# Kernel optimization log

Hardware: AMD Instinct MI355X
Metric: run time of the kernel (lower is better)

## Reference

```python
import jax, jax.numpy as jnp
import numpy as np

B, N, D_IN = 8, 1024, 512
H, D_HEAD = 8, 64
D_EXPAND, D_OUT = 2048, 512
D_Q = D_HEAD * H            # 512
D_V = D_IN * H              # 4096
D_QKV = 2 * D_Q + D_V       # 5120
EPS = 1e-5


def setup_inputs() -> dict:
    key = jax.random.key(0)
    ks = jax.random.split(key, 16)
    s = 0.02
    return {
        "x": jax.random.normal(ks[0], (B, N, D_IN), jnp.float32),
        "pos_enc": jax.random.normal(ks[1], (1, N, D_IN), jnp.float32),
        "gamma1": jnp.ones((1, 1, D_IN), jnp.float32),
        "beta1": jnp.zeros((1, 1, D_IN), jnp.float32),
        "scale": jnp.asarray(1.414, jnp.float32),
        "W_qkv": jax.random.normal(ks[2], (D_IN, D_QKV), jnp.float32) * s,
        "b_qkv": jax.random.normal(ks[3], (D_QKV,), jnp.float32) * s,
        "W_merge": jax.random.normal(ks[4], (D_V, D_IN), jnp.float32) * s,
        "b_merge": jax.random.normal(ks[5], (D_IN,), jnp.float32) * s,
        "gamma2": jnp.ones((1, 1, D_IN), jnp.float32),
        "beta2": jnp.zeros((1, 1, D_IN), jnp.float32),
        "W1": jax.random.normal(ks[6], (D_IN, D_EXPAND), jnp.float32) * s,
        "b1": jax.random.normal(ks[7], (D_EXPAND,), jnp.float32) * s,
        "gamma3": jnp.ones((1, 1, D_EXPAND), jnp.float32),
        "beta3": jnp.zeros((1, 1, D_EXPAND), jnp.float32),
        "W2": jax.random.normal(ks[8], (D_EXPAND, D_OUT), jnp.float32) * s,
        "b2": jax.random.normal(ks[9], (D_OUT,), jnp.float32) * s,
    }


def _feature_norm(x, gamma, beta):
    # torch FeatureNorm: stats over dim=1 (sequence dim), unbiased=False
    mean = x.mean(axis=1, keepdims=True)
    var = x.var(axis=1, keepdims=True)
    return gamma * (x - mean) / jnp.sqrt(var + EPS) + beta


def _swish(x):
    return x * jax.nn.sigmoid(x)


def reference(x, pos_enc, gamma1, beta1, scale, W_qkv, b_qkv, W_merge, b_merge,
              gamma2, beta2, W1, b1, gamma3, beta3, W2, b2):
    Bs, Ns, _ = x.shape
    h = _feature_norm(x, gamma1, beta1) + pos_enc
    qkv = _swish(h) @ W_qkv + b_qkv                      # (B, N, D_QKV)
    q = qkv[..., :D_Q].reshape(Bs, Ns, H, D_HEAD).transpose(0, 2, 1, 3)        # (B,H,N,dh)
    k = qkv[..., D_Q:2 * D_Q].reshape(Bs, Ns, H, D_HEAD).transpose(0, 2, 1, 3)
    v = qkv[..., 2 * D_Q:].reshape(Bs, Ns, H, D_IN).transpose(0, 2, 1, 3)      # (B,H,N,d_in)
    # squared euclidean distance via |q|^2 + |k|^2 - 2 q.k
    q2 = jnp.sum(q * q, axis=-1)                         # (B,H,N)
    k2 = jnp.sum(k * k, axis=-1)                         # (B,H,N)
    qk = jnp.einsum('bhnc,bhmc->bhnm', q, k)             # (B,H,N,N)
    d2 = jnp.maximum(q2[..., :, None] + k2[..., None, :] - 2.0 * qk, 0.0)
    score = jnp.exp(-d2 / (scale * scale))               # RBF kernel, no softmax
    out = jnp.einsum('bhnm,bhmc->bhnc', score, v)        # (B,H,N,d_in)
    out = out.transpose(0, 2, 1, 3).reshape(Bs, Ns, H * D_IN)
    x2 = x + out @ W_merge + b_merge                     # merge heads + residual
    ffh = _feature_norm(x2, gamma2, beta2) @ W1 + b1
    ffh = _swish(_feature_norm(ffh, gamma3, beta3))
    ff = ffh @ W2 + b2
    return ff + x2                                        # shortcut is Identity (d_in == d_out)
```

## Files before the change

### kernel.cpp

```cpp
#include <hip/hip_runtime.h>
#include <hip/hip_bf16.h>
#include <stdint.h>

typedef __bf16 bf16_t;
typedef __bf16 bf16x8 __attribute__((ext_vector_type(8)));
typedef __bf16 bf16x4 __attribute__((ext_vector_type(4)));
typedef float f32x4 __attribute__((ext_vector_type(4)));

__global__ void transp_kernel(const float* __restrict__ in, bf16_t* __restrict__ out,
                              int K, int N) {
  __shared__ float tile[32][33];
  int k0 = blockIdx.x * 32, n0 = blockIdx.y * 32;
  int tx = threadIdx.x, ty = threadIdx.y;
#pragma unroll
  for (int i = 0; i < 4; i++)
    tile[ty + 8 * i][tx] = in[(size_t)(k0 + ty + 8 * i) * N + n0 + tx];
  __syncthreads();
#pragma unroll
  for (int i = 0; i < 4; i++)
    out[(size_t)(n0 + ty + 8 * i) * K + k0 + tx] = (bf16_t)tile[tx][ty + 8 * i];
}

#define NSPLIT 16

template <typename T>
__global__ __launch_bounds__(256) void norm_partial(
    const T* __restrict__ in, float* __restrict__ part, int D) {
  const int nd = D >> 7;
  const int bid = blockIdx.x;
  const int s = bid % NSPLIT;
  const int rem = bid / NSPLIT;
  const int dc = rem % nd;
  const int b = rem / nd;
  const int t = threadIdx.x;
  const int d = (dc << 7) + (t & 127);
  const int half = t >> 7;
  const int rows = 1024 / NSPLIT;
  const T* base = in + ((size_t)b * 1024 + s * rows) * D + d;
  float sum = 0.f, sq = 0.f;
  for (int n = half; n < rows; n += 2) {
    float v = (float)base[(size_t)n * D];
    sum += v;
    sq += v * v;
  }
  __shared__ float r0[256], r1[256];
  r0[t] = sum;
  r1[t] = sq;
  __syncthreads();
  if (t < 128) {
    float ssum = r0[t] + r0[t + 128];
    float ssq = r1[t] + r1[t + 128];
    size_t col = (size_t)b * D + (dc << 7) + t;
    part[col * (2 * NSPLIT) + s] = ssum;
    part[col * (2 * NSPLIT) + NSPLIT + s] = ssq;
  }
}

__global__ __launch_bounds__(256) void norm_stats(
    const float* __restrict__ part, float2* __restrict__ stats, int total) {
  int col = blockIdx.x * 256 + threadIdx.x;
  if (col >= total) return;
  const float* p = part + (size_t)col * (2 * NSPLIT);
  float sum = 0.f, sq = 0.f;
#pragma unroll
  for (int s = 0; s < NSPLIT; s++) {
    sum += p[s];
    sq += p[NSPLIT + s];
  }
  float mean = sum * (1.f / 1024.f);
  float var = sq * (1.f / 1024.f) - mean * mean;
  stats[col] = make_float2(mean, rsqrtf(var + 1e-5f));
}

template <int MODE, typename T>
__global__ __launch_bounds__(256) void norm_apply(
    const T* __restrict__ in, const float2* __restrict__ stats,
    const float* __restrict__ gamma, const float* __restrict__ beta,
    const float* __restrict__ pos, bf16_t* __restrict__ out, int logD) {
  const int D = 1 << logD;
  size_t idx = ((size_t)blockIdx.x * 256 + threadIdx.x) * 4;
  int d = (int)(idx & (D - 1));
  size_t row = idx >> logD;
  int b = (int)(row >> 10);
  int n = (int)(row & 1023);
  float vv[4];
  if constexpr (sizeof(T) == 4) {
    float4 v = *(const float4*)(in + idx);
    vv[0] = v.x; vv[1] = v.y; vv[2] = v.z; vv[3] = v.w;
  } else {
    bf16x4 v = *(const bf16x4*)(in + idx);
#pragma unroll
    for (int j = 0; j < 4; j++) vv[j] = (float)v[j];
  }
  float4 g = *(const float4*)(gamma + d);
  float4 be = *(const float4*)(beta + d);
  const float2* st = stats + (size_t)b * D + d;
  float gg[4] = {g.x, g.y, g.z, g.w};
  float bb[4] = {be.x, be.y, be.z, be.w};
  float pp[4] = {0.f, 0.f, 0.f, 0.f};
  if (MODE == 1) {
    float4 p = *(const float4*)(pos + (size_t)n * D + d);
    pp[0] = p.x; pp[1] = p.y; pp[2] = p.z; pp[3] = p.w;
  }
  bf16x4 o;
#pragma unroll
  for (int j = 0; j < 4; j++) {
    float2 s = st[j];
    float h = gg[j] * (vv[j] - s.x) * s.y + bb[j];
    if (MODE == 1) h += pp[j];
    if (MODE == 1 || MODE == 3) h = h / (1.f + __expf(-h));
    o[j] = (bf16_t)h;
  }
  *(bf16x4*)(out + idx) = o;
}

__global__ __launch_bounds__(256) void combine2(
    const float* __restrict__ p0, const float* __restrict__ p1,
    const float* __restrict__ bias, const float* __restrict__ res,
    float* __restrict__ out) {
  size_t idx = ((size_t)blockIdx.x * 256 + threadIdx.x) * 4;
  int col = (int)(idx & 511);
  float4 a = *(const float4*)(p0 + idx);
  float4 b = *(const float4*)(p1 + idx);
  float4 rr = *(const float4*)(res + idx);
  float4 bi = *(const float4*)(bias + col);
  float4 o;
  o.x = a.x + b.x + rr.x + bi.x;
  o.y = a.y + b.y + rr.y + bi.y;
  o.z = a.z + b.z + rr.z + bi.z;
  o.w = a.w + b.w + rr.w + bi.w;
  *(float4*)(out + idx) = o;
}

enum { EPI_QKV = 0, EPI_RAW = 1, EPI_BF16 = 2 };

template <int EPI, int SPLITK>
__global__ void __launch_bounds__(256, 2) gemm_bf16(
    const bf16_t* __restrict__ A, const bf16_t* __restrict__ Bt,
    const float* __restrict__ bias,
    void* __restrict__ out0, bf16_t* __restrict__ out1,
    int M, int N, int K) {
  __shared__ bf16_t smem[2 * 128 * 64];
  bf16_t* sA = smem;
  bf16_t* sB = smem + 128 * 64;
  const int nwg = gridDim.x;
  int wg = blockIdx.x;
  wg = (wg & 7) * (nwg >> 3) + (wg >> 3);
  int kslice = 0;
  if (SPLITK) {
    int half = nwg >> 1;
    kslice = (wg >= half) ? 1 : 0;
    wg -= kslice * half;
  }
  const int mt = M >> 7;
  const int bm = wg % mt;
  const int bn = wg / mt;
  const int t = threadIdx.x;
  const int w = t >> 6, l = t & 63;
  const int wm = w >> 1, wn = w & 1;
  const int lrow = l >> 3;
  const int lcol = (l & 7) ^ lrow;

  f32x4 acc[4][4];
  const f32x4 z4 = {0.f, 0.f, 0.f, 0.f};
#pragma unroll
  for (int m = 0; m < 4; m++)
#pragma unroll
    for (int n = 0; n < 4; n++) acc[m][n] = z4;

  const bf16_t* Asrc = A + (size_t)(bm * 128 + w * 32 + lrow) * K + lcol * 8;
  const bf16_t* Bsrc = Bt + (size_t)(bn * 128 + w * 32 + lrow) * K + lcol * 8;

  const int kbeg = SPLITK ? kslice * (K >> 1) : 0;
  const int kend = kbeg + (SPLITK ? (K >> 1) : K);
  for (int kk = kbeg; kk < kend; kk += 64) {
#pragma unroll
    for (int i = 0; i < 4; i++) {
      __builtin_amdgcn_global_load_lds(
          (const __attribute__((address_space(1))) void*)(const void*)(Asrc + (size_t)i * 8 * K + kk),
          (__attribute__((address_space(3))) void*)(void*)((char*)sA + (w * 4 + i) * 1024),
          16, 0, 0);
      __builtin_amdgcn_global_load_lds(
          (const __attribute__((address_space(1))) void*)(const void*)(Bsrc + (size_t)i * 8 * K + kk),
          (__attribute__((address_space(3))) void*)(void*)((char*)sB + (w * 4 + i) * 1024),
          16, 0, 0);
    }
    __syncthreads();
#pragma unroll
    for (int ks = 0; ks < 2; ks++) {
      bf16x8 af[4], bfr[4];
      const int lc = ks * 4 + (l >> 4);
#pragma unroll
      for (int m = 0; m < 4; m++) {
        int row = wm * 64 + m * 16 + (l & 15);
        af[m] = *(const bf16x8*)((const char*)sA + row * 128 + ((lc ^ (row & 7)) << 4));
      }
#pragma unroll
      for (int n = 0; n < 4; n++) {
        int row = wn * 64 + n * 16 + (l & 15);
        bfr[n] = *(const bf16x8*)((const char*)sB + row * 128 + ((lc ^ (row & 7)) << 4));
      }
      __builtin_amdgcn_s_setprio(1);
#pragma unroll
      for (int m = 0; m < 4; m++)
#pragma unroll
        for (int n = 0; n < 4; n++)
          acc[m][n] = __builtin_amdgcn_mfma_f32_16x16x32_bf16(af[m], bfr[n], acc[m][n], 0, 0, 0);
      __builtin_amdgcn_s_setprio(0);
    }
    __syncthreads();
  }

  const int rowbase = bm * 128 + wm * 64 + ((l >> 4) << 2);
  const int colbase = bn * 128 + wn * 64 + (l & 15);
#pragma unroll
  for (int m = 0; m < 4; m++) {
#pragma unroll
    for (int n = 0; n < 4; n++) {
      int row = rowbase + m * 16;
      int col = colbase + n * 16;
      if (EPI == EPI_QKV) {
        float bc = bias[col];
        if (col < 1024) {
          bf16_t* qkb = (bf16_t*)out0;
#pragma unroll
          for (int r = 0; r < 4; r++)
            qkb[(size_t)(row + r) * 1024 + col] = (bf16_t)(acc[m][n][r] + bc);
        } else {
          int c2 = col - 1024;
          int hh = c2 >> 9, vc = c2 & 511;
          int bidx = row >> 10, nidx = row & 1023;
          bf16x4 pk;
#pragma unroll
          for (int r = 0; r < 4; r++) pk[r] = (bf16_t)(acc[m][n][r] + bc);
          *(bf16x4*)(out1 + ((size_t)((bidx << 3) + hh) * 512 + vc) * 1024 + nidx) = pk;
        }
      } else if (EPI == EPI_RAW) {
        float* o = (float*)out0 + (size_t)kslice * M * N;
#pragma unroll
        for (int r = 0; r < 4; r++) o[(size_t)(row + r) * N + col] = acc[m][n][r];
      } else {
        float bc = bias[col];
#pragma unroll
        for (int r = 0; r < 4; r++)
          out1[(size_t)(row + r) * N + col] = (bf16_t)(acc[m][n][r] + bc);
      }
    }
  }
}

__global__ void q2k2_kernel(const bf16_t* __restrict__ qk, float* __restrict__ q2,
                            float* __restrict__ k2) {
  int tid = blockIdx.x * 256 + threadIdx.x;
  int b = tid >> 13;
  int h = (tid >> 10) & 7;
  int n = tid & 1023;
  const bf16_t* row = qk + (size_t)((b << 10) + n) * 1024 + (h << 6);
  float sq = 0.f, sk = 0.f;
#pragma unroll
  for (int i = 0; i < 8; i++) {
    bf16x8 vq = *(const bf16x8*)(row + i * 8);
    bf16x8 vk = *(const bf16x8*)(row + 512 + i * 8);
#pragma unroll
    for (int j = 0; j < 8; j++) {
      float fq = (float)vq[j];
      sq += fq * fq;
      float fk = (float)vk[j];
      sk += fk * fk;
    }
  }
  q2[tid] = sq;
  k2[tid] = sk;
}

__global__ void __launch_bounds__(512, 2) attn_kernel(
    const bf16_t* __restrict__ qk, const bf16_t* __restrict__ vt,
    const float* __restrict__ q2, const float* __restrict__ k2,
    const float* __restrict__ scale_p, bf16_t* __restrict__ attn_out) {
  __shared__ bf16_t s_lds[64 * 64];
  const int blk = blockIdx.x;
  const int bh = (blk & 7) * 8 + (blk >> 7);
  const int mtile = (blk >> 3) & 15;
  const int b = bh >> 3, h = bh & 7;
  const int t = threadIdx.x, w = t >> 6, l = t & 63;
  const int wq = w >> 2;
  const int wv = w & 3;
  const float sc = scale_p[0];
  const float minus_inv = -1.f / (sc * sc);

  const bf16_t* qbase =
      qk + ((size_t)((b << 10) + (mtile << 6) + (wq << 5))) * 1024 + (h << 6);
  bf16x8 qf[2][2];
#pragma unroll
  for (int it = 0; it < 2; it++)
#pragma unroll
    for (int kc = 0; kc < 2; kc++)
      qf[it][kc] = *(const bf16x8*)(qbase + (size_t)(it * 16 + (l & 15)) * 1024 +
                                    kc * 32 + ((l >> 4) << 3));
  float q2r[2];
  const float* q2base = q2 + (bh << 10) + (mtile << 6) + (wq << 5);
#pragma unroll
  for (int it = 0; it < 2; it++) q2r[it] = q2base[it * 16 + (l & 15)];

  f32x4 acc[2][8];
  const f32x4 z4 = {0.f, 0.f, 0.f, 0.f};
#pragma unroll
  for (int m = 0; m < 2; m++)
#pragma unroll
    for (int nn = 0; nn < 8; nn++) acc[m][nn] = z4;

  const bf16_t* kbase = qk + ((size_t)(b << 10)) * 1024 + 512 + (h << 6);
  const bf16_t* vbase = vt + ((size_t)(bh << 9)) * 1024;
  const float* k2base = k2 + (bh << 10);

#pragma unroll 1
  for (int kt = 0; kt < 16; kt++) {
    float k2r[4];
#pragma unroll
    for (int r = 0; r < 4; r++)
      k2r[r] = k2base[kt * 64 + wv * 16 + ((l >> 4) << 2) + r];
    f32x4 sacc[2];
#pragma unroll
    for (int it = 0; it < 2; it++) sacc[it] = z4;
#pragma unroll
    for (int kc = 0; kc < 2; kc++) {
      bf16x8 kf = *(const bf16x8*)(kbase + (size_t)(kt * 64 + wv * 16 + (l & 15)) * 1024 +
                                   kc * 32 + ((l >> 4) << 3));
#pragma unroll
      for (int it = 0; it < 2; it++)
        sacc[it] = __builtin_amdgcn_mfma_f32_16x16x32_bf16(kf, qf[it][kc], sacc[it], 0, 0, 0);
    }
    __syncthreads();
#pragma unroll
    for (int it = 0; it < 2; it++) {
      int i = (wq << 5) + it * 16 + (l & 15);
      bf16x4 pk;
#pragma unroll
      for (int r = 0; r < 4; r++) {
        float d2 = fmaxf(q2r[it] + k2r[r] - 2.f * sacc[it][r], 0.f);
        pk[r] = (bf16_t)__expf(d2 * minus_inv);
      }
      int jc8 = (wv << 2) + (l >> 4);
      *(bf16x4*)((char*)s_lds + i * 128 + ((jc8 ^ ((i & 7) << 1)) << 3)) = pk;
    }
    __syncthreads();
#pragma unroll
    for (int kc = 0; kc < 2; kc++) {
      bf16x8 sf[2];
#pragma unroll
      for (int m = 0; m < 2; m++) {
        int i = (wq << 5) + m * 16 + (l & 15);
        int jcA = (kc << 3) + ((l >> 4) << 1);
        sf[m] = *(const bf16x8*)((const char*)s_lds + i * 128 +
                                 ((jcA ^ ((i & 7) << 1)) << 3));
      }
#pragma unroll
      for (int half = 0; half < 2; half++) {
        bf16x8 vf[4];
#pragma unroll
        for (int nb = 0; nb < 4; nb++)
          vf[nb] = *(const bf16x8*)(vbase +
                                    (size_t)(wv * 128 + (half * 4 + nb) * 16 + (l & 15)) * 1024 +
                                    kt * 64 + (kc << 5) + ((l >> 4) << 3));
        __builtin_amdgcn_s_setprio(1);
#pragma unroll
        for (int nb = 0; nb < 4; nb++)
#pragma unroll
          for (int m = 0; m < 2; m++)
            acc[m][half * 4 + nb] =
                __builtin_amdgcn_mfma_f32_16x16x32_bf16(sf[m], vf[nb], acc[m][half * 4 + nb], 0, 0, 0);
        __builtin_amdgcn_s_setprio(0);
      }
    }
  }
#pragma unroll
  for (int m = 0; m < 2; m++) {
    int nidx = (mtile << 6) + (wq << 5) + m * 16 + ((l >> 4) << 2);
#pragma unroll
    for (int nn = 0; nn < 8; nn++) {
      int col = (h << 9) + wv * 128 + nn * 16 + (l & 15);
      bf16_t* o = attn_out + ((size_t)((b << 10) + nidx)) * 4096 + col;
#pragma unroll
      for (int r = 0; r < 4; r++) o[(size_t)r * 4096] = (bf16_t)acc[m][nn][r];
    }
  }
}

extern "C" void kernel_launch(void* const* d_in, const int* in_sizes, int n_in,
                              void* d_out, int out_size, void* d_ws, size_t ws_size,
                              hipStream_t stream) {
  const float* x    = (const float*)d_in[0];
  const float* pos  = (const float*)d_in[1];
  const float* g1   = (const float*)d_in[2];
  const float* be1  = (const float*)d_in[3];
  const float* scl  = (const float*)d_in[4];
  const float* Wqkv = (const float*)d_in[5];
  const float* bqkv = (const float*)d_in[6];
  const float* Wmrg = (const float*)d_in[7];
  const float* bmrg = (const float*)d_in[8];
  const float* g2   = (const float*)d_in[9];
  const float* be2  = (const float*)d_in[10];
  const float* W1   = (const float*)d_in[11];
  const float* b1   = (const float*)d_in[12];
  const float* g3   = (const float*)d_in[13];
  const float* be3  = (const float*)d_in[14];
  const float* W2   = (const float*)d_in[15];
  const float* b2   = (const float*)d_in[16];
  float* outp = (float*)d_out;

  char* ws = (char*)d_ws;
  size_t off = 0;
  auto alloc = [&](size_t bytes) {
    char* p = ws + off;
    off += (bytes + 255) & ~(size_t)255;
    return p;
  };
  bf16_t* wtq = (bf16_t*)alloc(5120ull * 512 * 2);
  bf16_t* wtm = (bf16_t*)alloc(512ull * 4096 * 2);
  bf16_t* wt1 = (bf16_t*)alloc(2048ull * 512 * 2);
  bf16_t* wt2 = (bf16_t*)alloc(512ull * 2048 * 2);
  float*  q2  = (float*)alloc(65536ull * 4);
  float*  k2  = (float*)alloc(65536ull * 4);
  float*  prt = (float*)alloc(16384ull * 2 * NSPLIT * 4);
  float2* sts = (float2*)alloc(16384ull * 8);
  bf16_t* swh = (bf16_t*)alloc(8192ull * 512 * 2);
  bf16_t* qkb = (bf16_t*)alloc(8192ull * 1024 * 2);
  float*  x2b = (float*)alloc(8192ull * 512 * 4);
  bf16_t* x2n = (bf16_t*)alloc(8192ull * 512 * 2);
  bf16_t* atn = (bf16_t*)alloc(8192ull * 4096 * 2);
  bf16_t* vtb = (bf16_t*)alloc(64ull * 512 * 1024 * 2);
  float*  pmg = (float*)vtb;
  bf16_t* ffh = (bf16_t*)vtb;
  float*  pff = (float*)(vtb + 8192ull * 2048);
  bf16_t* ffn = (bf16_t*)atn;

  dim3 tb(32, 8);
  transp_kernel<<<dim3(512 / 32, 5120 / 32), tb, 0, stream>>>(Wqkv, wtq, 512, 5120);
  transp_kernel<<<dim3(4096 / 32, 512 / 32), tb, 0, stream>>>(Wmrg, wtm, 4096, 512);
  transp_kernel<<<dim3(512 / 32, 2048 / 32), tb, 0, stream>>>(W1, wt1, 512, 2048);
  transp_kernel<<<dim3(2048 / 32, 512 / 32), tb, 0, stream>>>(W2, wt2, 2048, 512);

  norm_partial<float><<<8 * 4 * NSPLIT, 256, 0, stream>>>(x, prt, 512);
  norm_stats<<<16, 256, 0, stream>>>(prt, sts, 8 * 512);
  norm_apply<1, float><<<4096, 256, 0, stream>>>(x, sts, g1, be1, pos, swh, 9);

  gemm_bf16<EPI_QKV, 0><<<64 * 40, 256, 0, stream>>>(swh, wtq, bqkv,
                                                     (void*)qkb, vtb, 8192, 5120, 512);
  q2k2_kernel<<<256, 256, 0, stream>>>(qkb, q2, k2);
  attn_kernel<<<1024, 512, 0, stream>>>(qkb, vtb, q2, k2, scl, atn);

  gemm_bf16<EPI_RAW, 1><<<2 * 64 * 4, 256, 0, stream>>>(atn, wtm, nullptr,
                                                        (void*)pmg, nullptr, 8192, 512, 4096);
  combine2<<<4096, 256, 0, stream>>>(pmg, pmg + 8192ull * 512, bmrg, x, x2b);

  norm_partial<float><<<8 * 4 * NSPLIT, 256, 0, stream>>>(x2b, prt, 512);
  norm_stats<<<16, 256, 0, stream>>>(prt, sts, 8 * 512);
  norm_apply<2, float><<<4096, 256, 0, stream>>>(x2b, sts, g2, be2, nullptr, x2n, 9);

  gemm_bf16<EPI_BF16, 0><<<64 * 16, 256, 0, stream>>>(x2n, wt1, b1,
                                                      nullptr, ffh, 8192, 2048, 512);

  norm_partial<bf16_t><<<8 * 16 * NSPLIT, 256, 0, stream>>>(ffh, prt, 2048);
  norm_stats<<<64, 256, 0, stream>>>(prt, sts, 8 * 2048);
  norm_apply<3, bf16_t><<<16384, 256, 0, stream>>>(ffh, sts, g3, be3, nullptr, ffn, 11);

  gemm_bf16<EPI_RAW, 1><<<2 * 64 * 4, 256, 0, stream>>>(ffn, wt2, nullptr,
                                                        (void*)pff, nullptr, 8192, 512, 2048);
  combine2<<<4096, 256, 0, stream>>>(pff, pff + 8192ull * 512, b2, x2b, outp);
}
```

Baseline: 672.4 us.

## Shrink attention tile to 32 query rows with 4-wave blocks

Each attention block drops from 8 waves over 64 query rows to 4 waves over 32 query rows, and the grid doubles to 2048 blocks with launch bounds of 256 threads and 3 blocks per CU. The V-operand loads are merged into a single batch of 8 fragments per k-chunk instead of two halves of 4. The aim is better occupancy and less barrier cost per block. In exchange, every K and V tile is fetched from global memory by twice as many blocks, which raises memory traffic.

Result: faster. 646.0 us (-3.9%).

```diff
diff --git a/kernel.cpp b/kernel.cpp
--- a/kernel.cpp
+++ b/kernel.cpp
@@ -273,23 +273,20 @@
   k2[tid] = sk;
 }
 
-__global__ void __launch_bounds__(512, 2) attn_kernel(
+__global__ void __launch_bounds__(256, 3) attn_kernel(
     const bf16_t* __restrict__ qk, const bf16_t* __restrict__ vt,
     const float* __restrict__ q2, const float* __restrict__ k2,
     const float* __restrict__ scale_p, bf16_t* __restrict__ attn_out) {
-  __shared__ bf16_t s_lds[64 * 64];
+  __shared__ bf16_t s_lds[32 * 64];
   const int blk = blockIdx.x;
-  const int bh = (blk & 7) * 8 + (blk >> 7);
-  const int mtile = (blk >> 3) & 15;
+  const int bh = (blk & 7) * 8 + (blk >> 8);
+  const int mtile = (blk >> 3) & 31;
   const int b = bh >> 3, h = bh & 7;
   const int t = threadIdx.x, w = t >> 6, l = t & 63;
-  const int wq = w >> 2;
-  const int wv = w & 3;
   const float sc = scale_p[0];
   const float minus_inv = -1.f / (sc * sc);
 
-  const bf16_t* qbase =
-      qk + ((size_t)((b << 10) + (mtile << 6) + (wq << 5))) * 1024 + (h << 6);
+  const bf16_t* qbase = qk + ((size_t)((b << 10) + (mtile << 5))) * 1024 + (h << 6);
   bf16x8 qf[2][2];
 #pragma unroll
   for (int it = 0; it < 2; it++)
@@ -298,7 +295,7 @@
       qf[it][kc] = *(const bf16x8*)(qbase + (size_t)(it * 16 + (l & 15)) * 1024 +
                                     kc * 32 + ((l >> 4) << 3));
   float q2r[2];
-  const float* q2base = q2 + (bh << 10) + (mtile << 6) + (wq << 5);
+  const float* q2base = q2 + (bh << 10) + (mtile << 5);
 #pragma unroll
   for (int it = 0; it < 2; it++) q2r[it] = q2base[it * 16 + (l & 15)];
 
@@ -318,13 +315,13 @@
     float k2r[4];
 #pragma unroll
     for (int r = 0; r < 4; r++)
-      k2r[r] = k2base[kt * 64 + wv * 16 + ((l >> 4) << 2) + r];
+      k2r[r] = k2base[kt * 64 + w * 16 + ((l >> 4) << 2) + r];
     f32x4 sacc[2];
 #pragma unroll
     for (int it = 0; it < 2; it++) sacc[it] = z4;
 #pragma unroll
     for (int kc = 0; kc < 2; kc++) {
-      bf16x8 kf = *(const bf16x8*)(kbase + (size_t)(kt * 64 + wv * 16 + (l & 15)) * 1024 +
+      bf16x8 kf = *(const bf16x8*)(kbase + (size_t)(kt * 64 + w * 16 + (l & 15)) * 1024 +
                                    kc * 32 + ((l >> 4) << 3));
 #pragma unroll
       for (int it = 0; it < 2; it++)
@@ -333,14 +330,14 @@
     __syncthreads();
 #pragma unroll
     for (int it = 0; it < 2; it++) {
-      int i = (wq << 5) + it * 16 + (l & 15);
+      int i = it * 16 + (l & 15);
       bf16x4 pk;
 #pragma unroll
       for (int r = 0; r < 4; r++) {
         float d2 = fmaxf(q2r[it] + k2r[r] - 2.f * sacc[it][r], 0.f);
         pk[r] = (bf16_t)__expf(d2 * minus_inv);
       }
-      int jc8 = (wv << 2) + (l >> 4);
+      int jc8 = (w << 2) + (l >> 4);
       *(bf16x4*)((char*)s_lds + i * 128 + ((jc8 ^ ((i & 7) << 1)) << 3)) = pk;
     }
     __syncthreads();
@@ -349,36 +346,31 @@
       bf16x8 sf[2];
 #pragma unroll
       for (int m = 0; m < 2; m++) {
-        int i = (wq << 5) + m * 16 + (l & 15);
+        int i = m * 16 + (l & 15);
         int jcA = (kc << 3) + ((l >> 4) << 1);
         sf[m] = *(const bf16x8*)((const char*)s_lds + i * 128 +
                                  ((jcA ^ ((i & 7) << 1)) << 3));
       }
-#pragma unroll
-      for (int half = 0; half < 2; half++) {
-        bf16x8 vf[4];
-#pragma unroll
-        for (int nb = 0; nb < 4; nb++)
-          vf[nb] = *(const bf16x8*)(vbase +
-                                    (size_t)(wv * 128 + (half * 4 + nb) * 16 + (l & 15)) * 1024 +
-                                    kt * 64 + (kc << 5) + ((l >> 4) << 3));
-        __builtin_amdgcn_s_setprio(1);
-#pragma unroll
-        for (int nb = 0; nb < 4; nb++)
-#pragma unroll
-          for (int m = 0; m < 2; m++)
-            acc[m][half * 4 + nb] =
-                __builtin_amdgcn_mfma_f32_16x16x32_bf16(sf[m], vf[nb], acc[m][half * 4 + nb], 0, 0, 0);
-        __builtin_amdgcn_s_setprio(0);
-      }
+      bf16x8 vf[8];
+#pragma unroll
+      for (int nn = 0; nn < 8; nn++)
+        vf[nn] = *(const bf16x8*)(vbase + (size_t)(w * 128 + nn * 16 + (l & 15)) * 1024 +
+                                  kt * 64 + (kc << 5) + ((l >> 4) << 3));
+      __builtin_amdgcn_s_setprio(1);
+#pragma unroll
+      for (int nn = 0; nn < 8; nn++)
+#pragma unroll
+        for (int m = 0; m < 2; m++)
+          acc[m][nn] = __builtin_amdgcn_mfma_f32_16x16x32_bf16(sf[m], vf[nn], acc[m][nn], 0, 0, 0);
+      __builtin_amdgcn_s_setprio(0);
     }
   }
 #pragma unroll
   for (int m = 0; m < 2; m++) {
-    int nidx = (mtile << 6) + (wq << 5) + m * 16 + ((l >> 4) << 2);
+    int nidx = (mtile << 5) + m * 16 + ((l >> 4) << 2);
 #pragma unroll
     for (int nn = 0; nn < 8; nn++) {
-      int col = (h << 9) + wv * 128 + nn * 16 + (l & 15);
+      int col = (h << 9) + w * 128 + nn * 16 + (l & 15);
       bf16_t* o = attn_out + ((size_t)((b << 10) + nidx)) * 4096 + col;
 #pragma unroll
       for (int r = 0; r < 4; r++) o[(size_t)r * 4096] = (bf16_t)acc[m][nn][r];
@@ -447,7 +439,7 @@
   gemm_bf16<EPI_QKV, 0><<<64 * 40, 256, 0, stream>>>(swh, wtq, bqkv,
                                                      (void*)qkb, vtb, 8192, 5120, 512);
   q2k2_kernel<<<256, 256, 0, stream>>>(qkb, q2, k2);
-  attn_kernel<<<1024, 512, 0, stream>>>(qkb, vtb, q2, k2, scl, atn);
+  attn_kernel<<<2048, 256, 0, stream>>>(qkb, vtb, q2, k2, scl, atn);
 
   gemm_bf16<EPI_RAW, 1><<<2 * 64 * 4, 256, 0, stream>>>(atn, wtm, nullptr,
                                                         (void*)pmg, nullptr, 8192, 512, 4096);
```
